# Kernel tuning notes

Measured on AMD Instinct MI355X. Metric: run time of the kernel, lower is better.

## Reference

```python
import jax, jax.numpy as jnp
import numpy as np

B, T, DIM = 2, 2048, 2048
H, HKV = 16, 4
D = DIM // H          # head_dim = 128
G = H // HKV          # GQA group = 4
ROPE_BASE = 10000.0
TRAIN_SEQ_LEN = 1024  # Rotary default; T > this triggers NTK base rescale


def _rope_tables():
    # Faithful to Rotary.forward: NTK scaling when seq_len > train_seq_len.
    if T > TRAIN_SEQ_LEN:
        sc = T / TRAIN_SEQ_LEN
        base = ROPE_BASE * sc ** (D / (D - 2))
    else:
        base = ROPE_BASE
    inv = 1.0 / base ** (np.arange(0, D, 2, dtype=np.float32) / D)  # [D/2]
    f = np.outer(np.arange(T, dtype=np.float32), inv)               # [T, D/2]
    cos = jnp.asarray(np.cos(f), jnp.float32)[None, :, None, :]     # [1,T,1,D/2]
    sin = jnp.asarray(np.sin(f), jnp.float32)[None, :, None, :]
    return cos, sin


def _rms_norm(x):
    # F.rms_norm with no weight: x / sqrt(mean(x^2) + eps), eps = finfo(dtype).eps
    eps = jnp.finfo(x.dtype).eps
    return x * jax.lax.rsqrt(jnp.mean(x * x, axis=-1, keepdims=True) + eps)


def _apply_rope(x, cos, sin):
    x1, x2 = jnp.split(x, 2, axis=-1)
    return jnp.concatenate([x1 * cos + x2 * sin, -x1 * sin + x2 * cos], axis=-1)


def setup_inputs() -> dict:
    key = jax.random.key(0)
    kx, kq, kk, kv, kp = jax.random.split(key, 5)
    s = lambda fan_in: 1.0 / np.sqrt(fan_in)
    kv_dim = HKV * D
    return {
        "x": jax.random.normal(kx, (B, T, DIM), jnp.float32),
        "Wq": jax.random.normal(kq, (DIM, DIM), jnp.float32) * s(DIM),
        "Wk": jax.random.normal(kk, (kv_dim, DIM), jnp.float32) * s(DIM),
        "Wv": jax.random.normal(kv, (kv_dim, DIM), jnp.float32) * s(DIM),
        "Wproj": jax.random.normal(kp, (DIM, DIM), jnp.float32) * s(DIM),
        "q_gain": jnp.full((H,), 1.0, jnp.float32),
    }


def reference(x, Wq, Wk, Wv, Wproj, q_gain):
    # QKV projections (bias-free linears)
    q = (x @ Wq.T).reshape(B, T, H, D)
    k = (x @ Wk.T).reshape(B, T, HKV, D)
    v = (x @ Wv.T).reshape(B, T, HKV, D)

    # QK RMSNorm + RoPE + per-head q gain
    q = _rms_norm(q)
    k = _rms_norm(k)
    cos, sin = _rope_tables()
    q = _apply_rope(q, cos, sin)
    k = _apply_rope(k, cos, sin)
    q = q * q_gain[None, None, :, None]

    # GQA causal SDPA without materializing repeated K/V:
    # group query heads by kv head: q -> [B,T,HKV,G,D]
    qg = q.reshape(B, T, HKV, G, D)
    scores = jnp.einsum('btkgd,bskd->bkgts', qg, k) / np.sqrt(D)  # [B,HKV,G,T,T]
    causal = jnp.tril(jnp.ones((T, T), bool))
    scores = jnp.where(causal[None, None, None], scores, -jnp.inf)
    p = jax.nn.softmax(scores, axis=-1)
    y = jnp.einsum('bkgts,bskd->btkgd', p, v).reshape(B, T, H, D)

    out = y.reshape(B, T, DIM) @ Wproj.T
    return out, v
```

## Files before the change

kernel.cpp:

```cpp
#include <hip/hip_runtime.h>
#include <hip/hip_bf16.h>

typedef __bf16 bf16_t;
typedef __bf16 bf16x4 __attribute__((ext_vector_type(4)));
typedef __bf16 bf16x8 __attribute__((ext_vector_type(8)));
typedef float f32x4 __attribute__((ext_vector_type(4)));

#define B_    2
#define T_    2048
#define DIM_  2048
#define H_    16
#define HKV_  4
#define D_    128
#define KVDIM_ 512

__device__ __forceinline__ bf16x8 cvt8(f32x4 a, f32x4 b) {
  bf16x8 r;
  r[0] = (bf16_t)a[0]; r[1] = (bf16_t)a[1]; r[2] = (bf16_t)a[2]; r[3] = (bf16_t)a[3];
  r[4] = (bf16_t)b[0]; r[5] = (bf16_t)b[1]; r[6] = (bf16_t)b[2]; r[7] = (bf16_t)b[3];
  return r;
}
__device__ __forceinline__ bf16x4 cvt4(f32x4 a) {
  bf16x4 r;
  r[0] = (bf16_t)a[0]; r[1] = (bf16_t)a[1]; r[2] = (bf16_t)a[2]; r[3] = (bf16_t)a[3];
  return r;
}
__device__ __forceinline__ void g2l16(const void* g, void* l) {
  __builtin_amdgcn_global_load_lds(
      (const __attribute__((address_space(1))) unsigned int*)g,
      (__attribute__((address_space(3))) unsigned int*)l, 16, 0, 0);
}

__global__ __launch_bounds__(256)
void cvt_all(const float* __restrict__ x,  const float* __restrict__ wq,
             const float* __restrict__ wk, const float* __restrict__ wv,
             const float* __restrict__ wp, bf16_t* __restrict__ xb,
             bf16_t* __restrict__ wqkvb, bf16_t* __restrict__ wpb) {
  int blk = blockIdx.x;
  const float* s; bf16_t* d; int lb;
  if (blk < 4096)      { s = x;  d = xb;                              lb = blk; }
  else if (blk < 6144) { s = wq; d = wqkvb;                           lb = blk - 4096; }
  else if (blk < 6656) { s = wk; d = wqkvb + (size_t)2048 * DIM_;     lb = blk - 6144; }
  else if (blk < 7168) { s = wv; d = wqkvb + (size_t)2560 * DIM_;     lb = blk - 6656; }
  else                 { s = wp; d = wpb;                             lb = blk - 7168; }
  size_t i = (size_t)lb * 2048 + (size_t)threadIdx.x * 8;
  f32x4 a = *(const f32x4*)(s + i);
  f32x4 b = *(const f32x4*)(s + i + 4);
  *(bf16x8*)(d + i) = cvt8(a, b);
}

template <int MODE, bool AASYNC, bool WASYNC>
__global__ __launch_bounds__(256)
void gemm128(const void* __restrict__ Ag, const void* __restrict__ Wg,
             const void* __restrict__ Wg2, void* __restrict__ Cb,
             bf16_t* __restrict__ Kb, bf16_t* __restrict__ Vb,
             float* __restrict__ Vf, int M, int N, int K) {
  constexpr int LDA = AASYNC ? 32 : 40;
  constexpr int LDW = WASYNC ? 32 : 40;
  __shared__ bf16_t As[128 * LDA];
  __shared__ bf16_t Ws[128 * LDW];
  const int tid  = threadIdx.x;
  const int wave = tid >> 6, lane = tid & 63;
  const int l16  = lane & 15, lg = lane >> 4;
  const int m0 = blockIdx.y * 128, n0 = blockIdx.x * 128;
  const int wm = (wave & 1) * 64, wn = (wave >> 1) * 64;
  f32x4 acc[4][4] = {};

  for (int k0 = 0; k0 < K; k0 += 32) {
    __syncthreads();
    if constexpr (AASYNC) {
      const bf16_t* A = (const bf16_t*)Ag;
      const int r = lane >> 2, c8 = (lane & 3) * 8;
      g2l16(&A[(size_t)(m0 + wave * 32 + r) * K + k0 + c8],      &As[(wave * 32) * LDA]);
      g2l16(&A[(size_t)(m0 + wave * 32 + 16 + r) * K + k0 + c8], &As[(wave * 32 + 16) * LDA]);
    } else {
      const float* A = (const float*)Ag;
#pragma unroll
      for (int j = 0; j < 4; j++) {
        int row = wave * 32 + j * 8 + (lane >> 3);
        int cf  = (lane & 7) * 4;
        f32x4 v = *(const f32x4*)&A[(size_t)(m0 + row) * K + k0 + cf];
        *(bf16x4*)&As[row * LDA + cf] = cvt4(v);
      }
    }
    if constexpr (WASYNC) {
      const bf16_t* W = (const bf16_t*)Wg;
      const int r = lane >> 2, c8 = (lane & 3) * 8;
      g2l16(&W[(size_t)(n0 + wave * 32 + r) * K + k0 + c8],      &Ws[(wave * 32) * LDW]);
      g2l16(&W[(size_t)(n0 + wave * 32 + 16 + r) * K + k0 + c8], &Ws[(wave * 32 + 16) * LDW]);
    } else {
      const float* W;
      int nb;
      if constexpr (MODE == 3) {
        if (n0 < 512) { W = (const float*)Wg;  nb = n0; }
        else          { W = (const float*)Wg2; nb = n0 - 512; }
      } else { W = (const float*)Wg; nb = n0; }
#pragma unroll
      for (int j = 0; j < 4; j++) {
        int row = wave * 32 + j * 8 + (lane >> 3);
        int cf  = (lane & 7) * 4;
        f32x4 v = *(const f32x4*)&W[(size_t)(nb + row) * K + k0 + cf];
        *(bf16x4*)&Ws[row * LDW + cf] = cvt4(v);
      }
    }
    __syncthreads();
    bf16x8 af[4], bfr[4];
#pragma unroll
    for (int i = 0; i < 4; i++)
      af[i] = *(const bf16x8*)&As[(wm + i * 16 + l16) * LDA + lg * 8];
#pragma unroll
    for (int j = 0; j < 4; j++)
      bfr[j] = *(const bf16x8*)&Ws[(wn + j * 16 + l16) * LDW + lg * 8];
#pragma unroll
    for (int i = 0; i < 4; i++)
#pragma unroll
      for (int j = 0; j < 4; j++)
        acc[i][j] = __builtin_amdgcn_mfma_f32_16x16x32_bf16(af[i], bfr[j], acc[i][j], 0, 0, 0);
  }
#pragma unroll
  for (int i = 0; i < 4; i++)
#pragma unroll
    for (int j = 0; j < 4; j++) {
      int row = m0 + wm + i * 16 + lg * 4;
      int col = n0 + wn + j * 16 + l16;
#pragma unroll
      for (int r = 0; r < 4; r++) {
        float v = acc[i][j][r];
        if constexpr (MODE == 0) {
          ((bf16_t*)Cb)[(size_t)(row + r) * N + col] = (bf16_t)v;
        } else if constexpr (MODE == 2) {
          ((float*)Cb)[(size_t)(row + r) * N + col] = v;
        } else if constexpr (MODE == 1) {
          if (col < 2048)      ((bf16_t*)Cb)[(size_t)(row + r) * 2048 + col] = (bf16_t)v;
          else if (col < 2560) Kb[(size_t)(row + r) * 512 + (col - 2048)] = (bf16_t)v;
          else {
            int c = col - 2560;
            Vb[(size_t)(row + r) * 512 + c] = (bf16_t)v;
            Vf[(size_t)(row + r) * 512 + c] = v;
          }
        } else {
          if (col < 512) ((bf16_t*)Cb)[(size_t)(row + r) * 512 + col] = (bf16_t)v;
          else {
            int c = col - 512;
            Vb[(size_t)(row + r) * 512 + c] = (bf16_t)v;
            Vf[(size_t)(row + r) * 512 + c] = v;
          }
        }
      }
    }
}

__global__ __launch_bounds__(256)
void qk_norm_rope(bf16_t* __restrict__ Qp, bf16_t* __restrict__ Kp,
                  const float* __restrict__ gain) {
  const int lane = threadIdx.x & 63;
  int row = blockIdx.x * 4 + (threadIdx.x >> 6);
  bf16_t* Xp; int nh; bool ag;
  const int MQ = B_ * T_ * H_;
  if (row < MQ) { Xp = Qp; nh = H_;  ag = true; }
  else          { Xp = Kp; nh = HKV_; ag = false; row -= MQ; }
  const int h = row % nh;
  const int t = (row / nh) % T_;
  bf16_t* p = Xp + (size_t)row * D_;
  float x0 = (float)p[lane * 2 + 0];
  float x1 = (float)p[lane * 2 + 1];
  float ss = x0 * x0 + x1 * x1;
#pragma unroll
  for (int m = 32; m >= 1; m >>= 1) ss += __shfl_xor(ss, m);
  const float rn = rsqrtf(ss * (1.0f / 128.0f) + 1.1920929e-07f);
  x0 *= rn; x1 *= rn;
  const float y0 = __shfl_xor(x0, 32);
  const float y1 = __shfl_xor(x1, 32);
  const int i0 = (lane & 31) * 2;
  const float kfreq = -0.22349352180347601f;
  float s0, c0, s1, c1;
  float a0 = (float)t * exp2f(kfreq * (float)i0);
  float a1 = (float)t * exp2f(kfreq * (float)(i0 + 1));
  sincosf(a0, &s0, &c0);
  sincosf(a1, &s1, &c1);
  float o0, o1;
  if (lane < 32) { o0 = x0 * c0 + y0 * s0;  o1 = x1 * c1 + y1 * s1; }
  else           { o0 = x0 * c0 - y0 * s0;  o1 = x1 * c1 - y1 * s1; }
  if (ag) { float g = gain[h]; o0 *= g; o1 *= g; }
  p[lane * 2 + 0] = (bf16_t)o0;
  p[lane * 2 + 1] = (bf16_t)o1;
}

#define KLD 136
#define VLD 72
#define PLD 68

__global__ __launch_bounds__(256, 2)
void flash_attn(const bf16_t* __restrict__ Q, const bf16_t* __restrict__ Kg,
                const bf16_t* __restrict__ V, bf16_t* __restrict__ Y) {
  __shared__ bf16_t Ks[64 * KLD];
  __shared__ bf16_t Vs[D_ * VLD];
  __shared__ float  Ps[4][16 * PLD];
  const int tid  = threadIdx.x;
  const int wave = tid >> 6, lane = tid & 63;
  const int l16  = lane & 15, lg = lane >> 4;
  const int b = blockIdx.z, h = blockIdx.y;
  const int pi = blockIdx.x;
  const int hk = h >> 2;

  int qr[2];
  qr[0] = 64 * pi + 16 * wave;
  qr[1] = 64 * (31 - pi) + 16 * wave;

  bf16x8 qf[2][4];
#pragma unroll
  for (int mt = 0; mt < 2; mt++)
#pragma unroll
    for (int kk = 0; kk < 4; kk++)
      qf[mt][kk] = *(const bf16x8*)&Q[(((size_t)b * T_ + qr[mt] + l16) * H_ + h) * D_ + kk * 32 + lg * 8];

  f32x4 o[2][8] = {};
  float lsum[2][4] = {};
  const float C = 0.12752531f;

  const int sr = tid >> 4, sc = (tid & 15) * 8;
  const int sp2 = (tid & 31) * 2;
  const int dvh = (tid >> 5) * 8;

  bf16x8 kreg[4];
  bf16x8 vreg[2][2];
  auto pf_load = [&](int k0) {
#pragma unroll
    for (int j = 0; j < 4; j++)
      kreg[j] = *(const bf16x8*)&Kg[(((size_t)b * T_ + k0 + sr + 16 * j) * HKV_ + hk) * D_ + sc];
#pragma unroll
    for (int it = 0; it < 2; it++) {
      const bf16_t* vb = &V[(((size_t)b * T_ + k0 + sp2) * HKV_ + hk) * D_ + dvh + it * 64];
      vreg[it][0] = *(const bf16x8*)vb;
      vreg[it][1] = *(const bf16x8*)(vb + HKV_ * D_);
    }
  };
  auto pf_store = [&]() {
#pragma unroll
    for (int j = 0; j < 4; j++)
      *(bf16x8*)&Ks[(sr + 16 * j) * KLD + sc] = kreg[j];
#pragma unroll
    for (int it = 0; it < 2; it++) {
      int dd = dvh + it * 64;
      const unsigned short* au = (const unsigned short*)&vreg[it][0];
      const unsigned short* bu = (const unsigned short*)&vreg[it][1];
#pragma unroll
      for (int i = 0; i < 8; i++) {
        unsigned int pr = (unsigned int)au[i] | ((unsigned int)bu[i] << 16);
        *(unsigned int*)&Vs[(dd + i) * VLD + sp2] = pr;
      }
    }
  };

  const int nkb = 32 - pi;
  pf_load(0);
  for (int kb = 0; kb < nkb; kb++) {
    const int k0 = kb * 64;
    __syncthreads();
    pf_store();
    __syncthreads();
    if (kb + 1 < nkb) pf_load(k0 + 64);

    const bool act0 = (kb <= pi);

    f32x4 s[2][4] = {};
#pragma unroll
    for (int kk = 0; kk < 4; kk++) {
      bf16x8 kf[4];
#pragma unroll
      for (int f = 0; f < 4; f++)
        kf[f] = *(const bf16x8*)&Ks[(f * 16 + l16) * KLD + kk * 32 + lg * 8];
      if (act0)
#pragma unroll
        for (int f = 0; f < 4; f++)
          s[0][f] = __builtin_amdgcn_mfma_f32_16x16x32_bf16(qf[0][kk], kf[f], s[0][f], 0, 0, 0);
#pragma unroll
      for (int f = 0; f < 4; f++)
        s[1][f] = __builtin_amdgcn_mfma_f32_16x16x32_bf16(qf[1][kk], kf[f], s[1][f], 0, 0, 0);
    }
    bf16x8 pf[2][2];
    float* pw = Ps[wave];
#pragma unroll
    for (int mt = 0; mt < 2; mt++) {
      if (mt == 0 && !act0) continue;
      const bool diag = (mt == 0) ? (kb == pi) : (kb == nkb - 1);
      if (diag) {
        const int myq = qr[mt] + lg * 4;
#pragma unroll
        for (int f = 0; f < 4; f++)
#pragma unroll
          for (int r = 0; r < 4; r++) {
            int kcol = k0 + f * 16 + l16;
            float p = (kcol <= myq + r) ? exp2f(s[mt][f][r] * C) : 0.0f;
            lsum[mt][r] += p;
            pw[(lg * 4 + r) * PLD + f * 16 + l16] = p;
          }
      } else {
#pragma unroll
        for (int f = 0; f < 4; f++)
#pragma unroll
          for (int r = 0; r < 4; r++) {
            float p = exp2f(s[mt][f][r] * C);
            lsum[mt][r] += p;
            pw[(lg * 4 + r) * PLD + f * 16 + l16] = p;
          }
      }
      __threadfence_block();
      f32x4 pa0 = *(const f32x4*)&pw[l16 * PLD + lg * 8];
      f32x4 pa1 = *(const f32x4*)&pw[l16 * PLD + lg * 8 + 4];
      f32x4 pb0 = *(const f32x4*)&pw[l16 * PLD + 32 + lg * 8];
      f32x4 pb1 = *(const f32x4*)&pw[l16 * PLD + 32 + lg * 8 + 4];
      pf[mt][0] = cvt8(pa0, pa1);
      pf[mt][1] = cvt8(pb0, pb1);
      __threadfence_block();
    }
#pragma unroll
    for (int f = 0; f < 8; f++) {
      bf16x8 v0 = *(const bf16x8*)&Vs[(f * 16 + l16) * VLD + lg * 8];
      bf16x8 v1 = *(const bf16x8*)&Vs[(f * 16 + l16) * VLD + 32 + lg * 8];
      if (act0) {
        o[0][f] = __builtin_amdgcn_mfma_f32_16x16x32_bf16(pf[0][0], v0, o[0][f], 0, 0, 0);
        o[0][f] = __builtin_amdgcn_mfma_f32_16x16x32_bf16(pf[0][1], v1, o[0][f], 0, 0, 0);
      }
      o[1][f] = __builtin_amdgcn_mfma_f32_16x16x32_bf16(pf[1][0], v0, o[1][f], 0, 0, 0);
      o[1][f] = __builtin_amdgcn_mfma_f32_16x16x32_bf16(pf[1][1], v1, o[1][f], 0, 0, 0);
    }
  }
#pragma unroll
  for (int mt = 0; mt < 2; mt++) {
    float rl[4];
#pragma unroll
    for (int r = 0; r < 4; r++) {
      float l = lsum[mt][r];
      l += __shfl_xor(l, 1);
      l += __shfl_xor(l, 2);
      l += __shfl_xor(l, 4);
      l += __shfl_xor(l, 8);
      rl[r] = 1.0f / l;
    }
#pragma unroll
    for (int f = 0; f < 8; f++)
#pragma unroll
      for (int r = 0; r < 4; r++) {
        int t = qr[mt] + lg * 4 + r;
        Y[(((size_t)b * T_ + t) * H_ + h) * D_ + f * 16 + l16] = (bf16_t)(o[mt][f][r] * rl[r]);
      }
  }
}

extern "C" void kernel_launch(void* const* d_in, const int* in_sizes, int n_in,
                              void* d_out, int out_size, void* d_ws, size_t ws_size,
                              hipStream_t stream) {
  (void)in_sizes; (void)n_in; (void)out_size;
  const float* x     = (const float*)d_in[0];
  const float* Wq    = (const float*)d_in[1];
  const float* Wk    = (const float*)d_in[2];
  const float* Wv    = (const float*)d_in[3];
  const float* Wproj = (const float*)d_in[4];
  const float* qgain = (const float*)d_in[5];

  float* out  = (float*)d_out;
  float* vout = out + (size_t)B_ * T_ * DIM_;

  const size_t M = (size_t)B_ * T_;
  char* ws = (char*)d_ws;
  size_t off = 0;
  auto take = [&](size_t elems) { bf16_t* p = (bf16_t*)(ws + off); off += elems * sizeof(bf16_t); return p; };

  bf16_t* Qp = take(M * DIM_);
  bf16_t* Kp = take(M * KVDIM_);
  bf16_t* Vb = take(M * KVDIM_);

  const size_t cvt_elems = M * DIM_ + (size_t)3072 * DIM_ + (size_t)DIM_ * DIM_;
  const bool fast = (ws_size >= off + cvt_elems * sizeof(bf16_t));

  dim3 blk(256);
  if (fast) {
    bf16_t* xb     = take(M * DIM_);
    bf16_t* Wqkvb  = take((size_t)3072 * DIM_);
    bf16_t* Wpb    = take((size_t)DIM_ * DIM_);

    cvt_all<<<dim3(9216), blk, 0, stream>>>(x, Wq, Wk, Wv, Wproj, xb, Wqkvb, Wpb);

    gemm128<1, true, true><<<dim3(3072 / 128, M / 128), blk, 0, stream>>>(
        xb, Wqkvb, nullptr, Qp, Kp, Vb, vout, M, 3072, DIM_);

    qk_norm_rope<<<dim3((unsigned)((M * H_ + M * HKV_) / 4)), blk, 0, stream>>>(Qp, Kp, qgain);
    flash_attn<<<dim3(16, H_, B_), blk, 0, stream>>>(Qp, Kp, Vb, Qp);

    gemm128<2, true, true><<<dim3(DIM_ / 128, M / 128), blk, 0, stream>>>(
        Qp, Wpb, nullptr, out, nullptr, nullptr, nullptr, M, DIM_, DIM_);
  } else {
    gemm128<0, false, false><<<dim3(DIM_ / 128, M / 128), blk, 0, stream>>>(
        x, Wq, nullptr, Qp, nullptr, nullptr, nullptr, M, DIM_, DIM_);
    gemm128<3, false, false><<<dim3(2 * KVDIM_ / 128, M / 128), blk, 0, stream>>>(
        x, Wk, Wv, Kp, nullptr, Vb, vout, M, 2 * KVDIM_, DIM_);
    qk_norm_rope<<<dim3((unsigned)((M * H_ + M * HKV_) / 4)), blk, 0, stream>>>(Qp, Kp, qgain);
    flash_attn<<<dim3(16, H_, B_), blk, 0, stream>>>(Qp, Kp, Vb, Qp);
    gemm128<2, true, false><<<dim3(DIM_ / 128, M / 128), blk, 0, stream>>>(
        Qp, Wproj, nullptr, out, nullptr, nullptr, nullptr, M, DIM_, DIM_);
  }
}
```

Baseline: 350.7 us.

## Replace 128x128 GEMMs with 256x256-tile 8-wave pipelined GEMM kernel

Adds a gemm256 kernel with 256x256 output tiles, 512 threads and 128KB LDS double-buffered in half-tile stages. The schedule interleaves global-to-LDS prefetch with MFMA quadrants using explicit waitcnt, barriers and setprio. It is used for both the fused QKV projection and the output projection. The aim is more data reuse per loaded tile and better overlap of loads with compute, at the cost of far fewer blocks than CUs and heavy LDS use per block.

Result: faster. 317.6 us (-9.4%).

```diff
diff --git a/kernel.cpp b/kernel.cpp
--- a/kernel.cpp
+++ b/kernel.cpp
@@ -150,6 +150,155 @@
     }
 }
 
+#define SB() __builtin_amdgcn_sched_barrier(0)
+#define BARRIER() __builtin_amdgcn_s_barrier()
+#define LGKM0() do { asm volatile("s_waitcnt lgkmcnt(0)" ::: "memory"); SB(); } while (0)
+#define VMW(N) do { asm volatile("s_waitcnt vmcnt(" #N ")" ::: "memory"); SB(); } while (0)
+
+#define RD_A(BUF, QM) do { \
+  _Pragma("unroll") for (int f_ = 0; f_ < 4; f_++) { \
+    const int r_ = wm * 128 + (QM) * 64 + f_ * 16 + l16; \
+    _Pragma("unroll") for (int ks_ = 0; ks_ < 2; ks_++) \
+      a[f_][ks_] = *(const bf16x8*)(lds + (BUF) * 65536 + r_ * 128 + ((ks_ * 64 + lg * 16) ^ swz)); \
+  } } while (0)
+
+#define RD_B(BUF, QN, BB) do { \
+  _Pragma("unroll") for (int n_ = 0; n_ < 2; n_++) { \
+    const int r_ = wn * 64 + (QN) * 32 + n_ * 16 + l16; \
+    _Pragma("unroll") for (int ks_ = 0; ks_ < 2; ks_++) \
+      BB[n_][ks_] = *(const bf16x8*)(lds + (BUF) * 65536 + 32768 + r_ * 128 + ((ks_ * 64 + lg * 16) ^ swz)); \
+  } } while (0)
+
+#define MM(QM, QN, BB) do { \
+  __builtin_amdgcn_s_setprio(1); \
+  _Pragma("unroll") for (int f_ = 0; f_ < 4; f_++) \
+    _Pragma("unroll") for (int n_ = 0; n_ < 2; n_++) \
+      _Pragma("unroll") for (int ks_ = 0; ks_ < 2; ks_++) \
+        acc[(QM) * 4 + f_][(QN) * 2 + n_] = __builtin_amdgcn_mfma_f32_16x16x32_bf16( \
+            a[f_][ks_], BB[n_][ks_], acc[(QM) * 4 + f_][(QN) * 2 + n_], 0, 0, 0); \
+  __builtin_amdgcn_s_setprio(0); \
+  } while (0)
+
+#define K_ITER(KT0, LAST) do { \
+  const int kA1_ = ((KT0) + 1) * 64; \
+  const int kN2_ = ((KT0) + 2) * 64; \
+  const int kN3_ = ((KT0) + 3) * 64; \
+   \
+  RD_A(0, 0); RD_B(0, 0, b0); \
+  stage_half(Ag, m0, kA1_, 65536); \
+  asm volatile("s_waitcnt lgkmcnt(8)" ::: "memory"); \
+  SB(); BARRIER(); LGKM0(); \
+  MM(0, 0, b0); \
+  SB(); BARRIER(); \
+   \
+  RD_B(0, 1, b1); \
+  stage_half(Ag, m0 + 128, kA1_, 65536 + 16384); \
+  SB(); BARRIER(); LGKM0(); \
+  MM(0, 1, b1); \
+  SB(); BARRIER(); \
+   \
+  RD_A(0, 1); \
+  if (!(LAST)) stage_half(Wg, n0, kN2_, 32768); \
+  SB(); BARRIER(); LGKM0(); \
+  MM(1, 0, b0); \
+  SB(); BARRIER(); \
+   \
+  if (!(LAST)) { stage_half(Wg, n0 + 128, kN2_, 32768 + 16384); VMW(4); } \
+  else { VMW(0); } \
+  SB(); BARRIER(); \
+  MM(1, 1, b1); \
+  SB(); BARRIER(); \
+   \
+  RD_A(1, 0); RD_B(1, 0, b0); \
+  if (!(LAST)) stage_half(Ag, m0, kN2_, 0); \
+  asm volatile("s_waitcnt lgkmcnt(8)" ::: "memory"); \
+  SB(); BARRIER(); LGKM0(); \
+  MM(0, 0, b0); \
+  SB(); BARRIER(); \
+   \
+  RD_B(1, 1, b1); \
+  if (!(LAST)) stage_half(Ag, m0 + 128, kN2_, 16384); \
+  SB(); BARRIER(); LGKM0(); \
+  MM(0, 1, b1); \
+  SB(); BARRIER(); \
+   \
+  RD_A(1, 1); \
+  if (!(LAST)) stage_half(Wg, n0, kN3_, 65536 + 32768); \
+  SB(); BARRIER(); LGKM0(); \
+  MM(1, 0, b0); \
+  SB(); BARRIER(); \
+   \
+  if (!(LAST)) { stage_half(Wg, n0 + 128, kN3_, 65536 + 32768 + 16384); VMW(4); } \
+  SB(); BARRIER(); \
+  MM(1, 1, b1); \
+  SB(); BARRIER(); \
+} while (0)
+
+template <int MODE>
+__global__ __launch_bounds__(512, 2)
+void gemm256(const bf16_t* __restrict__ Ag, const bf16_t* __restrict__ Wg,
+             void* __restrict__ Cb, bf16_t* __restrict__ Kb, bf16_t* __restrict__ Vb,
+             float* __restrict__ Vf, int M, int N, int K) {
+  (void)M;
+  __shared__ __align__(16) char lds[131072];
+  const int tid  = threadIdx.x;
+  const int wave = tid >> 6, lane = tid & 63;
+  const int l16  = lane & 15, lg = lane >> 4;
+  const int wm = wave >> 2, wn = wave & 3;
+  const int swz = (l16 & 7) << 4;
+  const int m0 = blockIdx.y * 256, n0 = blockIdx.x * 256;
+  const int srow = lane >> 3;
+  const int scol = ((lane & 7) ^ srow) * 8;
+
+  auto stage_half = [&](const bf16_t* __restrict__ X, int xrow, int k0, int ldsoff) {
+    const bf16_t* src = X + (size_t)(xrow + wave * 16 + srow) * K + (k0 + scol);
+    char* dst = lds + ldsoff + wave * 2048;
+    g2l16(src, dst);
+    g2l16(src + (size_t)8 * K, dst + 1024);
+  };
+
+  f32x4 acc[8][4] = {};
+  bf16x8 a[4][2], b0[2][2], b1[2][2];
+
+  stage_half(Ag, m0,        0, 0);
+  stage_half(Ag, m0 + 128,  0, 16384);
+  stage_half(Wg, n0,        0, 32768);
+  stage_half(Wg, n0 + 128,  0, 32768 + 16384);
+  stage_half(Wg, n0,       64, 65536 + 32768);
+  stage_half(Wg, n0 + 128, 64, 65536 + 32768 + 16384);
+  VMW(4);
+  BARRIER();
+
+  const int NIT = K >> 7;
+  for (int it = 0; it < NIT - 1; ++it) {
+    K_ITER(2 * it, 0);
+  }
+  K_ITER(2 * (NIT - 1), 1);
+
+#pragma unroll
+  for (int mf = 0; mf < 8; mf++)
+#pragma unroll
+    for (int nf = 0; nf < 4; nf++) {
+      const int row = m0 + wm * 128 + mf * 16 + lg * 4;
+      const int col = n0 + wn * 64 + nf * 16 + l16;
+#pragma unroll
+      for (int r = 0; r < 4; r++) {
+        float v = acc[mf][nf][r];
+        if constexpr (MODE == 1) {
+          if (col < 2048)      ((bf16_t*)Cb)[(size_t)(row + r) * 2048 + col] = (bf16_t)v;
+          else if (col < 2560) Kb[(size_t)(row + r) * 512 + (col - 2048)] = (bf16_t)v;
+          else {
+            int c = col - 2560;
+            Vb[(size_t)(row + r) * 512 + c] = (bf16_t)v;
+            Vf[(size_t)(row + r) * 512 + c] = v;
+          }
+        } else {
+          ((float*)Cb)[(size_t)(row + r) * N + col] = v;
+        }
+      }
+    }
+}
+
 __global__ __launch_bounds__(256)
 void qk_norm_rope(bf16_t* __restrict__ Qp, bf16_t* __restrict__ Kp,
                   const float* __restrict__ gain) {
@@ -382,14 +531,14 @@
 
     cvt_all<<<dim3(9216), blk, 0, stream>>>(x, Wq, Wk, Wv, Wproj, xb, Wqkvb, Wpb);
 
-    gemm128<1, true, true><<<dim3(3072 / 128, M / 128), blk, 0, stream>>>(
-        xb, Wqkvb, nullptr, Qp, Kp, Vb, vout, M, 3072, DIM_);
+    gemm256<1><<<dim3(3072 / 256, M / 256), dim3(512), 0, stream>>>(
+        xb, Wqkvb, Qp, Kp, Vb, vout, (int)M, 3072, DIM_);
 
     qk_norm_rope<<<dim3((unsigned)((M * H_ + M * HKV_) / 4)), blk, 0, stream>>>(Qp, Kp, qgain);
     flash_attn<<<dim3(16, H_, B_), blk, 0, stream>>>(Qp, Kp, Vb, Qp);
 
-    gemm128<2, true, true><<<dim3(DIM_ / 128, M / 128), blk, 0, stream>>>(
-        Qp, Wpb, nullptr, out, nullptr, nullptr, nullptr, M, DIM_, DIM_);
+    gemm256<2><<<dim3(DIM_ / 256, M / 256), dim3(512), 0, stream>>>(
+        Qp, Wpb, out, nullptr, nullptr, nullptr, (int)M, DIM_, DIM_);
   } else {
     gemm128<0, false, false><<<dim3(DIM_ / 128, M / 128), blk, 0, stream>>>(
         x, Wq, nullptr, Qp, nullptr, nullptr, nullptr, M, DIM_, DIM_);
```
